# Kernel optimization log

Measured on AMD Instinct MI355X. Metric: run time of the kernel, lower is better.

The kernel has to match this reference:

```python
import jax, jax.numpy as jnp
import numpy as np

MARGIN = 0.2  # opt['loss']['margin']
EPS = 1e-12   # F.normalize eps default


def setup_inputs() -> dict:
    key = jax.random.key(0)
    k1, k2 = jax.random.split(key)
    B, D = 4096, 1024
    return {
        "image_features": jax.random.normal(k1, (B, D), dtype=jnp.float32),
        "text_features": jax.random.normal(k2, (B, D), dtype=jnp.float32),
    }


def _l2norm(x):
    # F.normalize(x, dim=1, p=2): x / max(||x||, eps)
    n = jnp.sqrt(jnp.sum(x * x, axis=1, keepdims=True))
    return x / jnp.maximum(n, EPS)


def reference(image_features, text_features):
    im = _l2norm(image_features)   # [B, D]
    tx = _l2norm(text_features)    # [B, D]
    # cosine similarity of unit vectors == dot product; single GEMM instead of
    # materializing the [B, B, D] expanded tensors the torch code builds.
    sim = im @ tx.T                # [B, B]
    diag = jnp.diagonal(sim)       # [B] positive-pair scores
    # VSE-style triplet (hinge) loss over all negatives, diagonal masked out.
    cost_s = jax.nn.relu(MARGIN + sim - diag[:, None])   # caption negatives
    cost_im = jax.nn.relu(MARGIN + sim - diag[None, :])  # image negatives
    off_diag = 1.0 - jnp.eye(sim.shape[0], dtype=sim.dtype)
    total_loss = jnp.sum((cost_s + cost_im) * off_diag)
    return total_loss, sim
```

## Files before the change

kernel.cpp:

```cpp
#include <hip/hip_runtime.h>
#include <hip/hip_bf16.h>

typedef unsigned short u16;
typedef __attribute__((ext_vector_type(8))) __bf16 bf16x8;
typedef __attribute__((ext_vector_type(4))) float f32x4;

#define B_SZ 4096
#define D_SZ 1024
#define MARGIN 0.2f

__device__ __forceinline__ u16 f2bf(float x) {
  __hip_bfloat16 h = __float2bfloat16(x);
  u16 r; __builtin_memcpy(&r, &h, 2); return r;
}

__global__ __launch_bounds__(256) void norm_diag_kernel(
    const float* __restrict__ im, const float* __restrict__ tx,
    u16* __restrict__ imn, u16* __restrict__ txn,
    float* __restrict__ diag, float* __restrict__ loss) {
  const int l = threadIdx.x & 63;
  const int row = blockIdx.x * 4 + (threadIdx.x >> 6);
  if (blockIdx.x == 0 && threadIdx.x == 0) *loss = 0.f;
  const size_t base = (size_t)row * D_SZ;
  const float4* pi4 = reinterpret_cast<const float4*>(im + base);
  const float4* pt4 = reinterpret_cast<const float4*>(tx + base);
  float4 vi[4], vt[4];
#pragma unroll
  for (int k = 0; k < 4; k++) { vi[k] = pi4[l + 64 * k]; vt[k] = pt4[l + 64 * k]; }
  float ssi = 0.f, sst = 0.f, dot = 0.f;
#pragma unroll
  for (int k = 0; k < 4; k++) {
    ssi += vi[k].x * vi[k].x + vi[k].y * vi[k].y + vi[k].z * vi[k].z + vi[k].w * vi[k].w;
    sst += vt[k].x * vt[k].x + vt[k].y * vt[k].y + vt[k].z * vt[k].z + vt[k].w * vt[k].w;
    dot += vi[k].x * vt[k].x + vi[k].y * vt[k].y + vi[k].z * vt[k].z + vi[k].w * vt[k].w;
  }
#pragma unroll
  for (int off = 32; off > 0; off >>= 1) {
    ssi += __shfl_xor(ssi, off, 64);
    sst += __shfl_xor(sst, off, 64);
    dot += __shfl_xor(dot, off, 64);
  }
  const float si = 1.0f / fmaxf(sqrtf(ssi), 1e-12f);
  const float st = 1.0f / fmaxf(sqrtf(sst), 1e-12f);
#pragma unroll
  for (int k = 0; k < 4; k++) {
    u16 oi[4] = { f2bf(vi[k].x * si), f2bf(vi[k].y * si),
                  f2bf(vi[k].z * si), f2bf(vi[k].w * si) };
    u16 ot[4] = { f2bf(vt[k].x * st), f2bf(vt[k].y * st),
                  f2bf(vt[k].z * st), f2bf(vt[k].w * st) };
    ushort4 pi, pt; __builtin_memcpy(&pi, oi, 8); __builtin_memcpy(&pt, ot, 8);
    reinterpret_cast<ushort4*>(imn + base)[l + 64 * k] = pi;
    reinterpret_cast<ushort4*>(txn + base)[l + 64 * k] = pt;
  }
  if (l == 0) diag[row] = dot * si * st;
}

__device__ __forceinline__ void gload_lds16(const u16* g, u16* l) {
  __builtin_amdgcn_global_load_lds((__attribute__((address_space(1))) void*)g,
                                   (__attribute__((address_space(3))) void*)l,
                                   16, 0, 0);
}

__global__ __launch_bounds__(1024, 4) void gemm_loss_kernel(
    const u16* __restrict__ A,
    const u16* __restrict__ Bt,
    const float* __restrict__ diag,
    float* __restrict__ sim,
    float* __restrict__ loss) {
  __shared__ u16 sm[65536];

  const int tid = threadIdx.x;
  const int l = tid & 63;
  const int w = tid >> 6;
  const int wr = w >> 2;
  const int wc = w & 3;
  const int ar = l & 15;
  const int arh = l >> 4;

  const int bid = blockIdx.x;
  const int s = (bid & 7) * 32 + (bid >> 3);
  const int tm = (s >> 4) * 256;
  const int tn = (s & 15) * 256;

  f32x4 acc[4][4] = {};

  const int l3 = l >> 3;
  const int cb = (l & 7) ^ l3;
  const int rho = w * 8 + l3;
  const u16* pR[4];
  pR[0] = A  + (size_t)(tm + rho)       * D_SZ + cb * 8;
  pR[1] = A  + (size_t)(tm + 128 + rho) * D_SZ + cb * 8;
  pR[2] = Bt + (size_t)(tn + rho)       * D_SZ + cb * 8;
  pR[3] = Bt + (size_t)(tn + 128 + rho) * D_SZ + cb * 8;

  const int sl0 = (arh ^ (ar & 7)) * 8;
  const int sl1 = ((4 + arh) ^ (ar & 7)) * 8;
  const int aOfs = ((wr & 1) * 64 + ar) * 64;
  const int bOfs = ((wc & 1) * 64 + ar) * 64;
  const int aReg = wr >> 1;
  const int bReg = 2 + (wc >> 1);

#pragma unroll
  for (int c = 0; c < 4; c++)
    gload_lds16(pR[c], sm + c * 8192 + w * 512);
  __syncthreads();

#pragma unroll 1
  for (int t = 0; t < 16; ++t) {
    const int buf = t & 1;
    if (t + 1 < 16) {
      const int nb = buf ^ 1;
      const int ko = (t + 1) * 64;
#pragma unroll
      for (int c = 0; c < 4; c++)
        gload_lds16(pR[c] + ko, sm + (nb * 4 + c) * 8192 + w * 512);
    }
    const u16* Ab = sm + (buf * 4 + aReg) * 8192 + aOfs;
    const u16* Bb = sm + (buf * 4 + bReg) * 8192 + bOfs;
    {
      bf16x8 af[4], bfr[4];
#pragma unroll
      for (int m = 0; m < 4; m++) af[m] = *(const bf16x8*)&Ab[m * 1024 + sl0];
#pragma unroll
      for (int n = 0; n < 4; n++) bfr[n] = *(const bf16x8*)&Bb[n * 1024 + sl0];
#pragma unroll
      for (int m = 0; m < 4; m++)
#pragma unroll
        for (int n = 0; n < 4; n++)
          acc[m][n] = __builtin_amdgcn_mfma_f32_16x16x32_bf16(af[m], bfr[n], acc[m][n], 0, 0, 0);
    }
    {
      bf16x8 af[4], bfr[4];
#pragma unroll
      for (int m = 0; m < 4; m++) af[m] = *(const bf16x8*)&Ab[m * 1024 + sl1];
#pragma unroll
      for (int n = 0; n < 4; n++) bfr[n] = *(const bf16x8*)&Bb[n * 1024 + sl1];
#pragma unroll
      for (int m = 0; m < 4; m++)
#pragma unroll
        for (int n = 0; n < 4; n++)
          acc[m][n] = __builtin_amdgcn_mfma_f32_16x16x32_bf16(af[m], bfr[n], acc[m][n], 0, 0, 0);
    }
    __syncthreads();
  }

  float dcs[4];
#pragma unroll
  for (int n = 0; n < 4; n++) dcs[n] = diag[tn + wc * 64 + n * 16 + ar];
  float lsum = 0.f;
#pragma unroll
  for (int m = 0; m < 4; m++) {
#pragma unroll
    for (int i = 0; i < 4; i++) {
      const int r = tm + wr * 64 + m * 16 + arh * 4 + i;
      const float dr = diag[r];
#pragma unroll
      for (int n = 0; n < 4; n++) {
        const int c = tn + wc * 64 + n * 16 + ar;
        const float s_ = acc[m][n][i];
        sim[(size_t)r * B_SZ + c] = s_;
        if (r != c)
          lsum += fmaxf(MARGIN + s_ - dr, 0.f) + fmaxf(MARGIN + s_ - dcs[n], 0.f);
      }
    }
  }
#pragma unroll
  for (int off = 32; off > 0; off >>= 1) lsum += __shfl_down(lsum, off, 64);

  float* wsum = (float*)sm;
  if (l == 0) wsum[w] = lsum;
  __syncthreads();
  if (tid == 0) {
    float tot = 0.f;
#pragma unroll
    for (int i = 0; i < 16; i++) tot += wsum[i];
    atomicAdd(loss, tot);
  }
}

extern "C" void kernel_launch(void* const* d_in, const int* in_sizes, int n_in,
                              void* d_out, int out_size, void* d_ws, size_t ws_size,
                              hipStream_t stream) {
  const float* im = (const float*)d_in[0];
  const float* tx = (const float*)d_in[1];
  float* out = (float*)d_out;
  float* loss = out;
  float* sim = out + 1;

  u16* imn = (u16*)d_ws;
  u16* txn = imn + (size_t)B_SZ * D_SZ;
  float* diag = (float*)(txn + (size_t)B_SZ * D_SZ);

  norm_diag_kernel<<<B_SZ / 4, 256, 0, stream>>>(im, tx, imn, txn, diag, loss);
  gemm_loss_kernel<<<(B_SZ / 256) * (B_SZ / 256), 1024, 0, stream>>>(imn, txn, diag, sim, loss);
}
```

Before: 51.87 us.

## Shrink GEMM tile to 256x128 with 512 threads and single-buffered LDS

Changes the GEMM block tile from 256x256 with 16 waves to 256x128 with 8 waves, doubling the grid to 512 blocks. The double-buffered LDS prefetch is replaced by a single buffer that loads and syncs each k-step, cutting LDS use to 48KB so more blocks can fit per CU. The aim is better CU balance and occupancy across 256 CUs, at the cost of losing load/compute overlap within a block and more global reloads of A. The two-stage sync is also a risk: the load for the next step may overwrite LDS before slower waves finish reading unless a trailing barrier remains.

```diff
diff --git a/kernel.cpp b/kernel.cpp
--- a/kernel.cpp
+++ b/kernel.cpp
@@ -61,62 +61,57 @@
                                    16, 0, 0);
 }
 
-__global__ __launch_bounds__(1024, 4) void gemm_loss_kernel(
+__global__ __launch_bounds__(512, 4) void gemm_loss_kernel(
     const u16* __restrict__ A,
     const u16* __restrict__ Bt,
     const float* __restrict__ diag,
     float* __restrict__ sim,
     float* __restrict__ loss) {
-  __shared__ u16 sm[65536];
+  __shared__ u16 sm[3 * 8192];
 
   const int tid = threadIdx.x;
   const int l = tid & 63;
   const int w = tid >> 6;
-  const int wr = w >> 2;
-  const int wc = w & 3;
+  const int wrM = w >> 1;
+  const int wcN = w & 1;
   const int ar = l & 15;
   const int arh = l >> 4;
 
   const int bid = blockIdx.x;
-  const int s = (bid & 7) * 32 + (bid >> 3);
-  const int tm = (s >> 4) * 256;
-  const int tn = (s & 15) * 256;
+  const int s = (bid & 7) * 64 + (bid >> 3);
+  const int tm = (s >> 5) * 256;
+  const int tn = (s & 31) * 128;
 
   f32x4 acc[4][4] = {};
 
   const int l3 = l >> 3;
   const int cb = (l & 7) ^ l3;
-  const int rho = w * 8 + l3;
-  const u16* pR[4];
-  pR[0] = A  + (size_t)(tm + rho)       * D_SZ + cb * 8;
-  pR[1] = A  + (size_t)(tm + 128 + rho) * D_SZ + cb * 8;
-  pR[2] = Bt + (size_t)(tn + rho)       * D_SZ + cb * 8;
-  pR[3] = Bt + (size_t)(tn + 128 + rho) * D_SZ + cb * 8;
+  const u16* pR[3][2];
+#pragma unroll
+  for (int c = 0; c < 2; c++) {
+    const int rr = w * 16 + c * 8 + l3;
+    pR[0][c] = A  + (size_t)(tm + rr)       * D_SZ + cb * 8;
+    pR[1][c] = A  + (size_t)(tm + 128 + rr) * D_SZ + cb * 8;
+    pR[2][c] = Bt + (size_t)(tn + rr)       * D_SZ + cb * 8;
+  }
 
   const int sl0 = (arh ^ (ar & 7)) * 8;
   const int sl1 = ((4 + arh) ^ (ar & 7)) * 8;
-  const int aOfs = ((wr & 1) * 64 + ar) * 64;
-  const int bOfs = ((wc & 1) * 64 + ar) * 64;
-  const int aReg = wr >> 1;
-  const int bReg = 2 + (wc >> 1);
-
-#pragma unroll
-  for (int c = 0; c < 4; c++)
-    gload_lds16(pR[c], sm + c * 8192 + w * 512);
-  __syncthreads();
+  const int aReg = wrM >> 1;
+  const int aOfs = ((wrM & 1) * 64 + ar) * 64;
+  const int bOfs = (wcN * 64 + ar) * 64;
 
 #pragma unroll 1
   for (int t = 0; t < 16; ++t) {
-    const int buf = t & 1;
-    if (t + 1 < 16) {
-      const int nb = buf ^ 1;
-      const int ko = (t + 1) * 64;
+    const int ko = t * 64;
 #pragma unroll
-      for (int c = 0; c < 4; c++)
-        gload_lds16(pR[c] + ko, sm + (nb * 4 + c) * 8192 + w * 512);
-    }
-    const u16* Ab = sm + (buf * 4 + aReg) * 8192 + aOfs;
-    const u16* Bb = sm + (buf * 4 + bReg) * 8192 + bOfs;
+    for (int rg = 0; rg < 3; rg++)
+#pragma unroll
+      for (int c = 0; c < 2; c++)
+        gload_lds16(pR[rg][c] + ko, sm + rg * 8192 + w * 1024 + c * 512);
+    __syncthreads();
+    const u16* Ab = sm + aReg * 8192 + aOfs;
+    const u16* Bb = sm + 2 * 8192 + bOfs;
     {
       bf16x8 af[4], bfr[4];
 #pragma unroll
@@ -146,17 +141,17 @@
 
   float dcs[4];
 #pragma unroll
-  for (int n = 0; n < 4; n++) dcs[n] = diag[tn + wc * 64 + n * 16 + ar];
+  for (int n = 0; n < 4; n++) dcs[n] = diag[tn + wcN * 64 + n * 16 + ar];
   float lsum = 0.f;
 #pragma unroll
   for (int m = 0; m < 4; m++) {
 #pragma unroll
     for (int i = 0; i < 4; i++) {
-      const int r = tm + wr * 64 + m * 16 + arh * 4 + i;
+      const int r = tm + wrM * 64 + m * 16 + arh * 4 + i;
       const float dr = diag[r];
 #pragma unroll
       for (int n = 0; n < 4; n++) {
-        const int c = tn + wc * 64 + n * 16 + ar;
+        const int c = tn + wcN * 64 + n * 16 + ar;
         const float s_ = acc[m][n][i];
         sim[(size_t)r * B_SZ + c] = s_;
         if (r != c)
@@ -173,7 +168,7 @@
   if (tid == 0) {
     float tot = 0.f;
 #pragma unroll
-    for (int i = 0; i < 16; i++) tot += wsum[i];
+    for (int i = 0; i < 8; i++) tot += wsum[i];
     atomicAdd(loss, tot);
   }
 }
@@ -192,5 +187,5 @@
   float* diag = (float*)(txn + (size_t)B_SZ * D_SZ);
 
   norm_diag_kernel<<<B_SZ / 4, 256, 0, stream>>>(im, tx, imn, txn, diag, loss);
-  gemm_loss_kernel<<<(B_SZ / 256) * (B_SZ / 256), 1024, 0, stream>>>(imn, txn, diag, sim, loss);
+  gemm_loss_kernel<<<(B_SZ / 256) * (B_SZ / 128), 512, 0, stream>>>(imn, txn, diag, sim, loss);
 }
```

After: 55.83 us. +7.6%, slower.
